# Optimization experiments

Hardware: AMD Instinct MI355X
Metric: run time of the kernel (lower is better)

Reference implementation:

```python
import math
import jax, jax.numpy as jnp
import numpy as np

B, H_IN, W_IN = 8, 16, 16
K, STRIDE = 3, 2
IN_CAPS, OUT_CAPS = 32, 32
P_SIZE, P_DIM = 16, 4
NUM_ROUTING = 3
EPS = 1e-8
LAMBDA_0, LAMBDA_DELTA = 0.001, 0.0001
LN_2PI = math.log(2.0 * math.pi)
C_IN = IN_CAPS * (P_SIZE + 1)  # 544


def setup_inputs() -> dict:
    key = jax.random.key(0)
    k1, k2 = jax.random.split(key)
    x = jax.random.uniform(k1, (B, H_IN, W_IN, C_IN), dtype=jnp.float32)
    # weights: [K*K*in_caps, out_caps, p_dim, p_dim] (leading 1 dim of torch param dropped)
    weights = jax.random.normal(k2, (K * K * IN_CAPS, OUT_CAPS, P_DIM, P_DIM), dtype=jnp.float32)
    beta_u = jnp.full((OUT_CAPS,), 0.1, dtype=jnp.float32)
    beta_a = jnp.full((OUT_CAPS,), 0.1, dtype=jnp.float32)
    return {"input_tensor": x, "weights": weights, "beta_u": beta_u, "beta_a": beta_a}


def _kernel_tile(x):
    # x: [B, H, W, C] -> [B, K, K, oh, ow, C]
    in_h, in_w = x.shape[1:3]
    end = in_w - K + 1
    tf = np.array([[s + k for s in range(0, end, STRIDE)] for k in range(K)])  # [K, out]
    out = x[:, tf]            # [B, K, oh, W, C]
    out = out[:, :, :, tf]    # [B, K, oh, K, ow, C]
    out = jnp.transpose(out, (0, 1, 3, 2, 4, 5))  # [B, K, K, oh, ow, C]
    oh = (in_h - K + 1) // STRIDE
    ow = (in_w - K + 1) // STRIDE
    return out, oh, ow


def _matrix_transform(poses, weights):
    # poses: [N, KKL, 16] -> votes: [N, KKL, out_caps, 16]
    n = poses.shape[0]
    p4 = poses.reshape(n, -1, P_DIM, P_DIM)
    votes = jnp.einsum('nkij,kojm->nkoim', p4, weights)
    return votes.reshape(n, -1, OUT_CAPS, P_SIZE)


def _m_step(act_in, r, votes, lam, beta_u, beta_a):
    r = r * act_in                                     # [N, KKL, out]
    r = r / (r.sum(axis=2, keepdims=True) + EPS)
    r_sum = r.sum(axis=1, keepdims=True)               # [N, 1, out]
    r_prob = (r / (r_sum + EPS))[..., None]            # [N, KKL, out, 1]
    mean = (r_prob * votes).sum(axis=1, keepdims=True)  # [N, 1, out, 16]
    std = jnp.sqrt((r_prob * (votes - mean) ** 2).sum(axis=1, keepdims=True) + EPS)
    r_sum_v = r_sum.reshape(-1, OUT_CAPS, 1)
    std_v = std.reshape(-1, OUT_CAPS, P_SIZE)
    cost = (beta_u[:, None] + jnp.log(std_v)) * r_sum_v
    act_out = jax.nn.sigmoid(lam * (beta_a - cost.sum(axis=-1)))  # [N, out]
    return act_out, mean, std_v[:, None]               # std: [N, 1, out, 16]


def _e_step(mean, std, act_out, votes):
    ln_p = -(votes - mean) ** 2 / (2.0 * std ** 2) - jnp.log(std) - LN_2PI / 2.0
    ln_ap = ln_p.sum(axis=3) + jnp.log(act_out.reshape(-1, 1, OUT_CAPS))
    return jax.nn.softmax(ln_ap, axis=-1)


def _em_routing(votes, act_in, beta_u, beta_a):
    n = votes.shape[0]
    r = jnp.full(votes.shape[:-1], 1.0 / OUT_CAPS, dtype=votes.dtype)
    lam = LAMBDA_0
    mean = act_out = None
    for t in range(NUM_ROUTING):
        lam += LAMBDA_DELTA
        act_out, mean, std = _m_step(act_in, r, votes, lam, beta_u, beta_a)
        if t < NUM_ROUTING - 1:
            r = _e_step(mean, std, act_out, votes)
    return mean, act_out


def reference(input_tensor, weights, beta_u, beta_a):
    bsz = input_tensor.shape[0]
    tiled, oh, ow = _kernel_tile(input_tensor)               # [B,K,K,oh,ow,544]
    # faithful row-major reshapes (match torch .contiguous().view)
    poses = tiled[..., :-IN_CAPS].reshape(-1, K * K * IN_CAPS, P_SIZE)
    acts = tiled[..., -IN_CAPS:].reshape(-1, K * K * IN_CAPS, 1)
    votes = _matrix_transform(poses, weights)                # [N, KKL, out, 16]
    mean, act_out = _em_routing(votes, acts, beta_u, beta_a)
    poses_out = mean.reshape(bsz, oh, ow, OUT_CAPS * P_SIZE)
    act_out = act_out.reshape(bsz, oh, ow, OUT_CAPS)
    return jnp.concatenate([poses_out, act_out], axis=-1)    # [B, oh, ow, 544]
```

## Files before the change

### kernel.cpp

```cpp
#include <hip/hip_runtime.h>


namespace {

constexpr int NKK = 288;
constexpr float EPSF = 1e-8f;
constexpr float LN2PI = 1.8378770664093453f;

typedef float v2f __attribute__((ext_vector_type(2)));

__device__ __forceinline__ float fastrcp(float x) { return __builtin_amdgcn_rcpf(x); }

__global__ __launch_bounds__(512, 4)
void caps_em_kernel(const float* __restrict__ x,
                    const float* __restrict__ Wg,
                    const float* __restrict__ bu,
                    const float* __restrict__ ba,
                    float* __restrict__ out)
{
    __shared__ float p4[NKK * 16];
    __shared__ float cIn[NKK];
    __shared__ float scr[8 * 32 * 33];
    __shared__ float meanS[32 * 18];
    __shared__ float i2vS[32 * 18];
    __shared__ float actS[32];
    __shared__ float baseS[32];

    const int n = blockIdx.x;
    const int t = threadIdx.x;

    for (int idx = t; idx < NKK * 16; idx += 512) {
        unsigned g = (unsigned)n * 4608u + (unsigned)idx;
        unsigned c = g & 511u, rest = g >> 9;
        unsigned ow = rest % 7u; rest /= 7u;
        unsigned oh = rest % 7u; rest /= 7u;
        unsigned kw = rest % 3u; rest /= 3u;
        unsigned kh = rest % 3u;
        unsigned b  = rest / 3u;
        p4[idx] = x[((b*16u + 2u*oh + kh)*16u + 2u*ow + kw)*544u + c];
    }
    for (int idx = t; idx < NKK; idx += 512) {
        unsigned g = (unsigned)n * 288u + (unsigned)idx;
        unsigned c = g & 31u, rest = g >> 5;
        unsigned ow = rest % 7u; rest /= 7u;
        unsigned oh = rest % 7u; rest /= 7u;
        unsigned kw = rest % 3u; rest /= 3u;
        unsigned kh = rest % 3u;
        unsigned b  = rest / 3u;
        const float a = x[((b*16u + 2u*oh + kh)*16u + 2u*ow + kw)*544u + 512u + c];
        cIn[idx] = a / (a + EPSF);
    }
    __syncthreads();

    const int o  = t & 31;
    const int kc = t >> 5;
    const int oo = t >> 4;
    const int pp = t & 15;

    float lam = 1.0e-3f;

    for (int it = 0; it < 3; ++it) {
        lam += 1.0e-4f;

        float S0 = 0.f;
        v2f Sv[8], Sq[8];
        #pragma unroll
        for (int q = 0; q < 8; ++q) { Sv[q] = (v2f)(0.f); Sq[q] = (v2f)(0.f); }

        if (it == 0) {
            #pragma unroll 2
            for (int kk = 0; kk < 18; ++kk) {
                const int k = kc*18 + kk;
                const float w = cIn[k] * 0.03125f;
                float P[16]; v2f W2[8];
                #pragma unroll
                for (int j = 0; j < 4; ++j) {
                    const float4 v4 = *(const float4*)&p4[k*16 + j*4];
                    P[j*4] = v4.x; P[j*4+1] = v4.y; P[j*4+2] = v4.z; P[j*4+3] = v4.w;
                    const float4 w4 = *(const float4*)&Wg[(k*32 + o)*16 + j*4];
                    W2[j*2]   = (v2f){w4.x, w4.y};
                    W2[j*2+1] = (v2f){w4.z, w4.w};
                }
                S0 += w;
                #pragma unroll
                for (int i = 0; i < 4; ++i) {
                    #pragma unroll
                    for (int m2 = 0; m2 < 2; ++m2) {
                        v2f v = P[i*4] * W2[m2];
                        v += P[i*4+1] * W2[2+m2];
                        v += P[i*4+2] * W2[4+m2];
                        v += P[i*4+3] * W2[6+m2];
                        const v2f wv = v * w;
                        Sv[i*2+m2] += wv;
                        Sq[i*2+m2] += wv * v;
                    }
                }
            }
        } else {
            v2f M2[8], I2[8];
            #pragma unroll
            for (int q = 0; q < 8; ++q) {
                M2[q] = *(const v2f*)&meanS[o*18 + q*2];
                I2[q] = *(const v2f*)&i2vS [o*18 + q*2];
            }
            const float base = baseS[o];
            #pragma unroll 2
            for (int kk = 0; kk < 18; ++kk) {
                const int k = kc*18 + kk;
                float P[16]; v2f W2[8];
                #pragma unroll
                for (int j = 0; j < 4; ++j) {
                    const float4 v4 = *(const float4*)&p4[k*16 + j*4];
                    P[j*4] = v4.x; P[j*4+1] = v4.y; P[j*4+2] = v4.z; P[j*4+3] = v4.w;
                    const float4 w4 = *(const float4*)&Wg[(k*32 + o)*16 + j*4];
                    W2[j*2]   = (v2f){w4.x, w4.y};
                    W2[j*2+1] = (v2f){w4.z, w4.w};
                }
                v2f vt[8];
                v2f sacc2 = (v2f)(0.f);
                #pragma unroll
                for (int i = 0; i < 4; ++i) {
                    #pragma unroll
                    for (int m2 = 0; m2 < 2; ++m2) {
                        v2f v = P[i*4] * W2[m2];
                        v += P[i*4+1] * W2[2+m2];
                        v += P[i*4+2] * W2[4+m2];
                        v += P[i*4+3] * W2[6+m2];
                        vt[i*2+m2] = v;
                        const v2f d = v - M2[i*2+m2];
                        sacc2 += (d * I2[i*2+m2]) * d;
                    }
                }
                const float lnp = base - (sacc2.x + sacc2.y);
                float mx = lnp;
                #pragma unroll
                for (int d = 1; d < 32; d <<= 1) mx = fmaxf(mx, __shfl_xor(mx, d, 64));
                const float e = __expf(lnp - mx);
                float ss = e;
                #pragma unroll
                for (int d = 1; d < 32; d <<= 1) ss += __shfl_xor(ss, d, 64);
                const float u = e * fastrcp(ss) * cIn[k];
                S0 += u;
                #pragma unroll
                for (int q = 0; q < 8; ++q) {
                    const v2f uv = vt[q] * u;
                    Sv[q] += uv;
                    Sq[q] += uv * vt[q];
                }
            }
        }

        S0 += __shfl_xor(S0, 32, 64);
        #pragma unroll
        for (int q = 0; q < 8; ++q) {
            Sv[q].x += __shfl_xor(Sv[q].x, 32, 64);
            Sv[q].y += __shfl_xor(Sv[q].y, 32, 64);
            Sq[q].x += __shfl_xor(Sq[q].x, 32, 64);
            Sq[q].y += __shfl_xor(Sq[q].y, 32, 64);
        }
        if ((kc & 1) == 0) {
            float* row = &scr[((kc >> 1)*32 + o)*33];
            #pragma unroll
            for (int q = 0; q < 8; ++q) {
                row[q*2]      = Sv[q].x; row[q*2+1]      = Sv[q].y;
                row[16 + q*2] = Sq[q].x; row[16 + q*2+1] = Sq[q].y;
            }
            row[32] = S0;
        }
        __syncthreads();

        {
            float sm = 0.f, s2 = 0.f, rs = 0.f;
            #pragma unroll
            for (int q = 0; q < 8; ++q) {
                const int b0 = (q*32 + oo)*33;
                sm += scr[b0 + pp];
                s2 += scr[b0 + 16 + pp];
                rs += scr[b0 + 32];
            }
            const float inv = 1.0f / (rs + EPSF);
            const float S1  = rs * inv;
            const float m   = sm * inv;
            float var = s2 * inv - m*m*(2.0f - S1);
            var = fmaxf(var, 0.0f) + EPSF;
            meanS[oo*18 + pp] = m;
            i2vS [oo*18 + pp] = 0.5f / var;
            float ls = 0.5f * __logf(var);
            #pragma unroll
            for (int d = 1; d < 16; d <<= 1) ls += __shfl_xor(ls, d, 64);
            if (pp == 0) {
                const float cost = (16.0f * bu[oo] + ls) * rs;
                const float ao   = 1.0f / (1.0f + __expf(-lam * (ba[oo] - cost)));
                actS[oo]  = ao;
                baseS[oo] = -ls - 8.0f*LN2PI + __logf(ao);
            }
        }
        __syncthreads();
    }

    for (int idx = t; idx < 544; idx += 512) {
        const float v = (idx < 512) ? meanS[(idx >> 4)*18 + (idx & 15)]
                                    : actS[idx - 512];
        out[n*544 + idx] = v;
    }
}

}

extern "C" void kernel_launch(void* const* d_in, const int* in_sizes, int n_in,
                              void* d_out, int out_size, void* d_ws, size_t ws_size,
                              hipStream_t stream) {
    (void)in_sizes; (void)n_in; (void)out_size; (void)d_ws; (void)ws_size;
    const float* x  = (const float*)d_in[0];
    const float* W  = (const float*)d_in[1];
    const float* bu = (const float*)d_in[2];
    const float* ba = (const float*)d_in[3];
    float* out = (float*)d_out;
    caps_em_kernel<<<dim3(392), dim3(512), 0, stream>>>(x, W, bu, ba, out);
}
```

Baseline: 130.1 us.

## Read poses directly from global memory and use DPP lane reductions

Removes the LDS staging buffer for pose patches. Each block now stores only per-k global offsets and loads pose float4s straight from global memory, relying on cache for the repeated reads across the three routing iterations. It also replaces the shfl_xor butterfly reductions with DPP and ds_swizzle sequences for the 32-lane softmax max/sum and the 16-lane log sum, and raises the unroll of the first-iteration loop to 3. The trade is fewer LDS bytes and a shorter prologue against more global/L2 traffic and latency inside the hot loops.

```diff
diff --git a/kernel.cpp b/kernel.cpp
--- a/kernel.cpp
+++ b/kernel.cpp
@@ -10,6 +10,35 @@
 typedef float v2f __attribute__((ext_vector_type(2)));
 
 __device__ __forceinline__ float fastrcp(float x) { return __builtin_amdgcn_rcpf(x); }
+
+template <int CTRL>
+__device__ __forceinline__ float dppf(float v) {
+    return __builtin_bit_cast(float,
+        __builtin_amdgcn_update_dpp(0, __builtin_bit_cast(int, v), CTRL, 0xF, 0xF, true));
+}
+__device__ __forceinline__ float swz16(float v) {
+    return __builtin_bit_cast(float,
+        __builtin_amdgcn_ds_swizzle(__builtin_bit_cast(int, v), 0x401F));
+}
+__device__ __forceinline__ float rmax32(float v) {
+    v = fmaxf(v, dppf<0xB1>(v));
+    v = fmaxf(v, dppf<0x4E>(v));
+    v = fmaxf(v, dppf<0x141>(v));
+    v = fmaxf(v, dppf<0x140>(v));
+    v = fmaxf(v, swz16(v));
+    return v;
+}
+__device__ __forceinline__ float rsum32(float v) {
+    v += dppf<0xB1>(v); v += dppf<0x4E>(v);
+    v += dppf<0x141>(v); v += dppf<0x140>(v);
+    v += swz16(v);
+    return v;
+}
+__device__ __forceinline__ float rsum16(float v) {
+    v += dppf<0xB1>(v); v += dppf<0x4E>(v);
+    v += dppf<0x141>(v); v += dppf<0x140>(v);
+    return v;
+}
 
 __global__ __launch_bounds__(512, 4)
 void caps_em_kernel(const float* __restrict__ x,
@@ -18,7 +47,7 @@
                     const float* __restrict__ ba,
                     float* __restrict__ out)
 {
-    __shared__ float p4[NKK * 16];
+    __shared__ unsigned koffS[NKK];
     __shared__ float cIn[NKK];
     __shared__ float scr[8 * 32 * 33];
     __shared__ float meanS[32 * 18];
@@ -29,26 +58,24 @@
     const int n = blockIdx.x;
     const int t = threadIdx.x;
 
-    for (int idx = t; idx < NKK * 16; idx += 512) {
-        unsigned g = (unsigned)n * 4608u + (unsigned)idx;
+    for (int k = t; k < NKK; k += 512) {
+        unsigned g = (unsigned)n * 4608u + (unsigned)(k * 16);
         unsigned c = g & 511u, rest = g >> 9;
         unsigned ow = rest % 7u; rest /= 7u;
         unsigned oh = rest % 7u; rest /= 7u;
         unsigned kw = rest % 3u; rest /= 3u;
         unsigned kh = rest % 3u;
         unsigned b  = rest / 3u;
-        p4[idx] = x[((b*16u + 2u*oh + kh)*16u + 2u*ow + kw)*544u + c];
-    }
-    for (int idx = t; idx < NKK; idx += 512) {
-        unsigned g = (unsigned)n * 288u + (unsigned)idx;
-        unsigned c = g & 31u, rest = g >> 5;
-        unsigned ow = rest % 7u; rest /= 7u;
-        unsigned oh = rest % 7u; rest /= 7u;
-        unsigned kw = rest % 3u; rest /= 3u;
-        unsigned kh = rest % 3u;
-        unsigned b  = rest / 3u;
-        const float a = x[((b*16u + 2u*oh + kh)*16u + 2u*ow + kw)*544u + 512u + c];
-        cIn[idx] = a / (a + EPSF);
+        koffS[k] = ((b*16u + 2u*oh + kh)*16u + 2u*ow + kw)*544u + c;
+        unsigned ga = (unsigned)n * 288u + (unsigned)k;
+        unsigned ca = ga & 31u; rest = ga >> 5;
+        ow = rest % 7u; rest /= 7u;
+        oh = rest % 7u; rest /= 7u;
+        kw = rest % 3u; rest /= 3u;
+        kh = rest % 3u;
+        b  = rest / 3u;
+        const float a = x[((b*16u + 2u*oh + kh)*16u + 2u*ow + kw)*544u + 512u + ca];
+        cIn[k] = a / (a + EPSF);
     }
     __syncthreads();
 
@@ -68,16 +95,18 @@
         for (int q = 0; q < 8; ++q) { Sv[q] = (v2f)(0.f); Sq[q] = (v2f)(0.f); }
 
         if (it == 0) {
-            #pragma unroll 2
+            #pragma unroll 3
             for (int kk = 0; kk < 18; ++kk) {
                 const int k = kc*18 + kk;
                 const float w = cIn[k] * 0.03125f;
+                const float* px = x + koffS[k];
+                const float* wp = Wg + (unsigned)k*512u + (unsigned)o*16u;
                 float P[16]; v2f W2[8];
                 #pragma unroll
                 for (int j = 0; j < 4; ++j) {
-                    const float4 v4 = *(const float4*)&p4[k*16 + j*4];
+                    const float4 v4 = *(const float4*)(px + j*4);
                     P[j*4] = v4.x; P[j*4+1] = v4.y; P[j*4+2] = v4.z; P[j*4+3] = v4.w;
-                    const float4 w4 = *(const float4*)&Wg[(k*32 + o)*16 + j*4];
+                    const float4 w4 = *(const float4*)(wp + j*4);
                     W2[j*2]   = (v2f){w4.x, w4.y};
                     W2[j*2+1] = (v2f){w4.z, w4.w};
                 }
@@ -107,12 +136,14 @@
             #pragma unroll 2
             for (int kk = 0; kk < 18; ++kk) {
                 const int k = kc*18 + kk;
+                const float* px = x + koffS[k];
+                const float* wp = Wg + (unsigned)k*512u + (unsigned)o*16u;
                 float P[16]; v2f W2[8];
                 #pragma unroll
                 for (int j = 0; j < 4; ++j) {
-                    const float4 v4 = *(const float4*)&p4[k*16 + j*4];
+                    const float4 v4 = *(const float4*)(px + j*4);
                     P[j*4] = v4.x; P[j*4+1] = v4.y; P[j*4+2] = v4.z; P[j*4+3] = v4.w;
-                    const float4 w4 = *(const float4*)&Wg[(k*32 + o)*16 + j*4];
+                    const float4 w4 = *(const float4*)(wp + j*4);
                     W2[j*2]   = (v2f){w4.x, w4.y};
                     W2[j*2+1] = (v2f){w4.z, w4.w};
                 }
@@ -132,14 +163,10 @@
                     }
                 }
                 const float lnp = base - (sacc2.x + sacc2.y);
-                float mx = lnp;
-                #pragma unroll
-                for (int d = 1; d < 32; d <<= 1) mx = fmaxf(mx, __shfl_xor(mx, d, 64));
-                const float e = __expf(lnp - mx);
-                float ss = e;
-                #pragma unroll
-                for (int d = 1; d < 32; d <<= 1) ss += __shfl_xor(ss, d, 64);
-                const float u = e * fastrcp(ss) * cIn[k];
+                const float mx = rmax32(lnp);
+                const float e  = __expf(lnp - mx);
+                const float ss = rsum32(e);
+                const float u  = e * fastrcp(ss) * cIn[k];
                 S0 += u;
                 #pragma unroll
                 for (int q = 0; q < 8; ++q) {
@@ -185,9 +212,7 @@
             var = fmaxf(var, 0.0f) + EPSF;
             meanS[oo*18 + pp] = m;
             i2vS [oo*18 + pp] = 0.5f / var;
-            float ls = 0.5f * __logf(var);
-            #pragma unroll
-            for (int d = 1; d < 16; d <<= 1) ls += __shfl_xor(ls, d, 64);
+            const float ls = rsum16(0.5f * __logf(var));
             if (pp == 0) {
                 const float cost = (16.0f * bu[oo] + ls) * rs;
                 const float ao   = 1.0f / (1.0f + __expf(-lam * (ba[oo] - cost)));
```

New measurement: 139.2 us. 7.0% more time.
